# Kernel tuning notes

Measured on AMD Instinct MI355X. Metric: run time of the kernel, lower is better.

Reference implementation:

```python
import jax, jax.numpy as jnp
import numpy as np


def setup_inputs() -> dict:
    key = jax.random.key(0)
    k1, k2 = jax.random.split(key)
    B, L, D = 8, 2048, 128
    x1 = jax.random.normal(k1, (B, L, D), dtype=jnp.float32)
    x2 = jax.random.normal(k2, (B, L, D), dtype=jnp.float32)
    return {"x1": x1, "x2": x2}


def reference(x1, x2):
    # attention[b, i, j] = <x1[b,i,:], x2[b,j,:]>   -> [B, L1, L2]
    attention = jnp.einsum("bid,bjd->bij", x1, x2)
    # softmax over axis=1 (rows / L1) and axis=2 (cols / L2)
    w_att_1 = jax.nn.softmax(attention, axis=1)              # [B, L1, L2]
    w_att_2 = jnp.swapaxes(jax.nn.softmax(attention, axis=2), 1, 2)  # [B, L2, L1]
    # Dot(axes=1): contract the sequence axis 1
    in1_aligned = jnp.einsum("bij,bid->bjd", w_att_1, x1)    # [B, L2, D]
    in2_aligned = jnp.einsum("bji,bjd->bid", w_att_2, x2)    # [B, L1, D]
    # submult(a, b) = concat([a - b, a * b]); combined = concat([a, b, a-b, a*b])
    q1_combined = jnp.concatenate(
        [x1, in2_aligned, x1 - in2_aligned, x1 * in2_aligned], axis=-1)  # [B, L1, 4D]
    q2_combined = jnp.concatenate(
        [x2, in1_aligned, x2 - in1_aligned, x2 * in1_aligned], axis=-1)  # [B, L2, 4D]
    return q1_combined, q2_combined
```

## Files before the change

### kernel.cpp

```cpp
#include <hip/hip_runtime.h>


typedef __bf16    bf16;
typedef _Float16  f16;
typedef __bf16    bf16x4 __attribute__((ext_vector_type(4)));
typedef _Float16  f16x4  __attribute__((ext_vector_type(4)));
typedef __bf16    bf16x8 __attribute__((ext_vector_type(8)));
typedef _Float16  f16x8  __attribute__((ext_vector_type(8)));
typedef float     floatx4 __attribute__((ext_vector_type(4)));
typedef unsigned int uintx4 __attribute__((ext_vector_type(4)));

#define NB 8
#define SL 2048
#define TI 64
#define NT 32

#define F16SZ (NB * SL * 128 * 2)

#define SKV_S  136
#define SVT_S  32

#define OFF_VT   8704
#define GSPAN    16896
#define OFF_L    33792
#define LDS_BYTES 34048

__global__ __launch_bounds__(256)
void prepass_cvt(const float* __restrict__ x1, const float* __restrict__ x2,
                 char* __restrict__ ws)
{
    __shared__ float tile[64 * 129];
    const int tid = threadIdx.x;
    const int j0  = blockIdx.x * 64;
    const int b   = blockIdx.y;
    const int z   = blockIdx.z;
    const float* src = z ? x2 : x1;
    f16*  oF = (f16*) (ws + (size_t)z * F16SZ);
    bf16* oT = (bf16*)(ws + 2 * (size_t)F16SZ + (size_t)z * F16SZ);

    #pragma unroll
    for (int n = 0; n < 8; ++n) {
        int ci = n * 256 + tid;
        int row = ci >> 5, c4 = ci & 31;
        const float4 v = *(const float4*)(src + ((size_t)b * SL + j0 + row) * 128 + c4 * 4);
        tile[row * 129 + c4 * 4 + 0] = v.x;
        tile[row * 129 + c4 * 4 + 1] = v.y;
        tile[row * 129 + c4 * 4 + 2] = v.z;
        tile[row * 129 + c4 * 4 + 3] = v.w;
        f16x4 h; h[0] = (f16)v.x; h[1] = (f16)v.y; h[2] = (f16)v.z; h[3] = (f16)v.w;
        *(f16x4*)(oF + ((size_t)b * SL + j0 + row) * 128 + c4 * 4) = h;
    }
    __syncthreads();
    #pragma unroll
    for (int n = 0; n < 8; ++n) {
        int fi = n * 256 + tid;
        int jg = fi & 15, d = fi >> 4;
        bf16x4 o;
        #pragma unroll
        for (int i = 0; i < 4; ++i) o[i] = (bf16)tile[(jg * 4 + i) * 129 + d];
        *(bf16x4*)(oT + ((size_t)b * 128 + d) * SL + j0 + jg * 4) = o;
    }
}

__global__ __launch_bounds__(256, 2)
void soft_attn_align_mfma(const float* __restrict__ x1,
                          const float* __restrict__ x2,
                          const char* __restrict__ ws,
                          float* __restrict__ out)
{
    __shared__ __align__(16) char lds_raw[LDS_BYTES];

    const int tid  = threadIdx.x;
    const int lane = tid & 63;
    const int wv   = tid >> 6;
    const int g    = wv >> 1;
    const int rowbase = (wv & 1) * 32;
    const int lr   = lane & 15;
    const int lq   = lane >> 4;
    const int t128 = tid & 127;

    char* gb   = lds_raw + g * GSPAN;
    f16*   sKV  = (f16*) (gb);
    bf16*  sVT  = (bf16*)(gb + OFF_VT);
    float* aOut = (float*)(lds_raw);
    float* sL   = (float*)(lds_raw + OFF_L);

    const int i0  = blockIdx.x * TI;
    const int bi  = blockIdx.y;
    const int dir = blockIdx.z;

    const float* xq = dir ? x2 : x1;
    const f16*  x1f = (const f16*)(ws);
    const f16*  x2f = (const f16*)(ws + F16SZ);
    const bf16* x1T = (const bf16*)(ws + 2 * (size_t)F16SZ);
    const bf16* x2T = (const bf16*)(ws + 3 * (size_t)F16SZ);
    const f16*  xqf  = dir ? x2f : x1f;
    const f16*  xkvf = dir ? x1f : x2f;
    const bf16* xvT  = dir ? x1T : x2T;

    f16x8 aQ[2][4];
    #pragma unroll
    for (int rb = 0; rb < 2; ++rb) {
        const f16* qrow = xqf + ((size_t)bi * SL + i0 + rowbase + rb * 16 + lr) * 128;
        #pragma unroll
        for (int kk = 0; kk < 4; ++kk)
            aQ[rb][kk] = *(const f16x8*)(qrow + kk * 32 + lq * 8);
    }

    float   l_acc[2] = {0.f, 0.f};
    floatx4 Oacc[2][8];
    #pragma unroll
    for (int rb = 0; rb < 2; ++rb)
        #pragma unroll
        for (int nd = 0; nd < 8; ++nd) Oacc[rb][nd] = (floatx4){0.f, 0.f, 0.f, 0.f};

    const int rowK = t128 >> 4, colK = t128 & 15;
    const int dV0  = t128 >> 2, jcV  = t128 & 3;
    const f16*  kvf = xkvf + ((size_t)bi * SL + g * 1024 + rowK) * 128 + colK * 8;
    const bf16* vTf = xvT + ((size_t)bi * 128 + dV0) * SL + g * 1024 + jcV * 8;

    f16x8  kreg[4];
    bf16x8 vreg[4];
    {
        #pragma unroll
        for (int n = 0; n < 4; ++n) {
            kreg[n] = *(const f16x8*)(kvf + (size_t)n * 8 * 128);
            vreg[n] = *(const bf16x8*)(vTf + (size_t)n * 32 * SL);
        }
    }

    for (int t = 0; t < NT; ++t) {
        __syncthreads();

        #pragma unroll
        for (int n = 0; n < 4; ++n) {
            *(f16x8*) (sKV + (rowK + n * 8) * SKV_S + colK * 8) = kreg[n];
            *(bf16x8*)(sVT + (dV0 + n * 32) * SVT_S + jcV * 8)  = vreg[n];
        }
        __syncthreads();

        if (t < NT - 1) {
            const f16*  kb = kvf + (size_t)(t + 1) * 32 * 128;
            const bf16* vb = vTf + (size_t)(t + 1) * 32;
            #pragma unroll
            for (int n = 0; n < 4; ++n) {
                kreg[n] = *(const f16x8*)(kb + (size_t)n * 8 * 128);
                vreg[n] = *(const bf16x8*)(vb + (size_t)n * 32 * SL);
            }
        }

        floatx4 Sf[2][2];
        Sf[0][0] = (floatx4){0.f,0.f,0.f,0.f}; Sf[0][1] = (floatx4){0.f,0.f,0.f,0.f};
        Sf[1][0] = (floatx4){0.f,0.f,0.f,0.f}; Sf[1][1] = (floatx4){0.f,0.f,0.f,0.f};
        __builtin_amdgcn_s_setprio(1);
        #pragma unroll
        for (int kk = 0; kk < 4; ++kk) {
            f16x8 aK0 = *(const f16x8*)(sKV + (lr)      * SKV_S + kk * 32 + lq * 8);
            f16x8 aK1 = *(const f16x8*)(sKV + (16 + lr) * SKV_S + kk * 32 + lq * 8);
            Sf[0][0] = __builtin_amdgcn_mfma_f32_16x16x32_f16(aK0, aQ[0][kk], Sf[0][0], 0, 0, 0);
            Sf[0][1] = __builtin_amdgcn_mfma_f32_16x16x32_f16(aK1, aQ[0][kk], Sf[0][1], 0, 0, 0);
            Sf[1][0] = __builtin_amdgcn_mfma_f32_16x16x32_f16(aK0, aQ[1][kk], Sf[1][0], 0, 0, 0);
            Sf[1][1] = __builtin_amdgcn_mfma_f32_16x16x32_f16(aK1, aQ[1][kk], Sf[1][1], 0, 0, 0);
        }
        __builtin_amdgcn_s_setprio(0);

        bf16x8 aP[2];
        #pragma unroll
        for (int rb = 0; rb < 2; ++rb) {
            float p00 = __expf(Sf[rb][0][0]), p01 = __expf(Sf[rb][0][1]);
            float p02 = __expf(Sf[rb][0][2]), p03 = __expf(Sf[rb][0][3]);
            float p10 = __expf(Sf[rb][1][0]), p11 = __expf(Sf[rb][1][1]);
            float p12 = __expf(Sf[rb][1][2]), p13 = __expf(Sf[rb][1][3]);
            l_acc[rb] += ((p00 + p01) + (p02 + p03)) + ((p10 + p11) + (p12 + p13));

            unsigned int A0, B0, A1, B1;
            asm("v_cvt_pk_bf16_f32 %0, %1, %2" : "=v"(A0) : "v"(p00), "v"(p01));
            asm("v_cvt_pk_bf16_f32 %0, %1, %2" : "=v"(B0) : "v"(p02), "v"(p03));
            asm("v_cvt_pk_bf16_f32 %0, %1, %2" : "=v"(A1) : "v"(p10), "v"(p11));
            asm("v_cvt_pk_bf16_f32 %0, %1, %2" : "=v"(B1) : "v"(p12), "v"(p13));
            asm("v_permlane32_swap_b32 %0, %1" : "+v"(A0), "+v"(A1));
            asm("v_permlane16_swap_b32 %0, %1" : "+v"(A0), "+v"(A1));
            asm("v_permlane32_swap_b32 %0, %1" : "+v"(B0), "+v"(B1));
            asm("v_permlane16_swap_b32 %0, %1" : "+v"(B0), "+v"(B1));
            uintx4 fr; fr.x = A0; fr.y = B0; fr.z = A1; fr.w = B1;
            aP[rb] = __builtin_bit_cast(bf16x8, fr);
        }

        __builtin_amdgcn_s_setprio(1);
        #pragma unroll
        for (int nd = 0; nd < 8; ++nd) {
            bf16x8 bV = *(const bf16x8*)(sVT + (nd * 16 + lr) * SVT_S + lq * 8);
            Oacc[0][nd] = __builtin_amdgcn_mfma_f32_16x16x32_bf16(aP[0], bV, Oacc[0][nd], 0, 0, 0);
            Oacc[1][nd] = __builtin_amdgcn_mfma_f32_16x16x32_bf16(aP[1], bV, Oacc[1][nd], 0, 0, 0);
        }
        __builtin_amdgcn_s_setprio(0);
    }

    float l_row[2][4];
    #pragma unroll
    for (int rb = 0; rb < 2; ++rb) {
        float lv = l_acc[rb];
        lv += __shfl_xor(lv, 16, 64);
        lv += __shfl_xor(lv, 32, 64);
        #pragma unroll
        for (int r = 0; r < 4; ++r)
            l_row[rb][r] = __shfl(lv, lq * 4 + r, 64);
    }

    __syncthreads();

    if (g == 1) {
        #pragma unroll
        for (int rb = 0; rb < 2; ++rb)
            #pragma unroll
            for (int r = 0; r < 4; ++r) {
                int row = rowbase + rb * 16 + lq * 4 + r;
                #pragma unroll
                for (int nd = 0; nd < 8; ++nd)
                    aOut[row * 132 + nd * 16 + lr] = Oacc[rb][nd][r];
                if (lr == 0) sL[row] = l_row[rb][r];
            }
    }
    __syncthreads();
    if (g == 0) {
        #pragma unroll
        for (int rb = 0; rb < 2; ++rb)
            #pragma unroll
            for (int r = 0; r < 4; ++r) {
                int row = rowbase + rb * 16 + lq * 4 + r;
                float inv = 1.0f / (l_row[rb][r] + sL[row]);
                #pragma unroll
                for (int nd = 0; nd < 8; ++nd) {
                    int idx = row * 132 + nd * 16 + lr;
                    aOut[idx] = (Oacc[rb][nd][r] + aOut[idx]) * inv;
                }
            }
    }
    __syncthreads();

    float* outb = out + ((size_t)dir * NB * SL + (size_t)bi * SL + i0) * 512;
    #pragma unroll
    for (int k = 0; k < 8; ++k) {
        int s = tid + 256 * k;
        int r = s >> 5, c4 = s & 31;
        float4 a = *(const float4*)(aOut + r * 132 + c4 * 4);
        float4 q = *(const float4*)(xq + ((size_t)bi * SL + i0 + r) * 128 + c4 * 4);
        float4 d, m;
        d.x = q.x - a.x; d.y = q.y - a.y; d.z = q.z - a.z; d.w = q.w - a.w;
        m.x = q.x * a.x; m.y = q.y * a.y; m.z = q.z * a.z; m.w = q.w * a.w;
        float4* orow = (float4*)(outb + (size_t)r * 512);
        orow[c4]      = q;
        orow[32 + c4] = a;
        orow[64 + c4] = d;
        orow[96 + c4] = m;
    }
}

extern "C" void kernel_launch(void* const* d_in, const int* in_sizes, int n_in,
                              void* d_out, int out_size, void* d_ws, size_t ws_size,
                              hipStream_t stream) {
    const float* x1 = (const float*)d_in[0];
    const float* x2 = (const float*)d_in[1];
    float* out = (float*)d_out;
    (void)in_sizes; (void)n_in; (void)out_size; (void)ws_size;

    dim3 pgrid(SL / 64, NB, 2);
    prepass_cvt<<<pgrid, dim3(256), 0, stream>>>(x1, x2, (char*)d_ws);

    dim3 grid(SL / TI, NB, 2);
    soft_attn_align_mfma<<<grid, dim3(256), 0, stream>>>(x1, x2, (const char*)d_ws, out);
}
```

Measured before the change: 130.6 us.

## Double-buffer K/V tiles in LDS to halve barriers per iteration

Adds a second LDS buffer for the K and V^T tiles so the next tile is written to shared memory while the current one is consumed, with global prefetch moved two tiles ahead. This cuts the loop to one __syncthreads per iteration instead of two. In exchange the LDS footprint roughly doubles, to about 67 KB per block, which may limit how many blocks can reside per CU alongside the launch bound of 2.

```diff
diff --git a/kernel.cpp b/kernel.cpp
--- a/kernel.cpp
+++ b/kernel.cpp
@@ -20,10 +20,11 @@
 #define SKV_S  136
 #define SVT_S  32
 
+#define BUFH     16896
+#define GSPAN    33792
 #define OFF_VT   8704
-#define GSPAN    16896
-#define OFF_L    33792
-#define LDS_BYTES 34048
+#define OFF_L    67584
+#define LDS_BYTES 67840
 
 __global__ __launch_bounds__(256)
 void prepass_cvt(const float* __restrict__ x1, const float* __restrict__ x2,
@@ -79,9 +80,11 @@
     const int lq   = lane >> 4;
     const int t128 = tid & 127;
 
-    char* gb   = lds_raw + g * GSPAN;
-    f16*   sKV  = (f16*) (gb);
-    bf16*  sVT  = (bf16*)(gb + OFF_VT);
+    char* gb = lds_raw + g * GSPAN;
+    f16*  sKV0 = (f16*) (gb);
+    bf16* sVT0 = (bf16*)(gb + OFF_VT);
+    f16*  sKV1 = (f16*) (gb + BUFH);
+    bf16* sVT1 = (bf16*)(gb + BUFH + OFF_VT);
     float* aOut = (float*)(lds_raw);
     float* sL   = (float*)(lds_raw + OFF_L);
 
@@ -121,27 +124,40 @@
 
     f16x8  kreg[4];
     bf16x8 vreg[4];
-    {
-        #pragma unroll
-        for (int n = 0; n < 4; ++n) {
-            kreg[n] = *(const f16x8*)(kvf + (size_t)n * 8 * 128);
-            vreg[n] = *(const bf16x8*)(vTf + (size_t)n * 32 * SL);
-        }
-    }
+
+    #pragma unroll
+    for (int n = 0; n < 4; ++n) {
+        kreg[n] = *(const f16x8*)(kvf + (size_t)n * 8 * 128);
+        vreg[n] = *(const bf16x8*)(vTf + (size_t)n * 32 * SL);
+    }
+    #pragma unroll
+    for (int n = 0; n < 4; ++n) {
+        *(f16x8*) (sKV0 + (rowK + n * 8) * SKV_S + colK * 8) = kreg[n];
+        *(bf16x8*)(sVT0 + (dV0 + n * 32) * SVT_S + jcV * 8)  = vreg[n];
+    }
+    #pragma unroll
+    for (int n = 0; n < 4; ++n) {
+        kreg[n] = *(const f16x8*)(kvf + 32 * 128 + (size_t)n * 8 * 128);
+        vreg[n] = *(const bf16x8*)(vTf + 32 + (size_t)n * 32 * SL);
+    }
+    __syncthreads();
 
     for (int t = 0; t < NT; ++t) {
-        __syncthreads();
-
-        #pragma unroll
-        for (int n = 0; n < 4; ++n) {
-            *(f16x8*) (sKV + (rowK + n * 8) * SKV_S + colK * 8) = kreg[n];
-            *(bf16x8*)(sVT + (dV0 + n * 32) * SVT_S + jcV * 8)  = vreg[n];
-        }
-        __syncthreads();
+        f16*  sKVc = (t & 1) ? sKV1 : sKV0;
+        bf16* sVTc = (t & 1) ? sVT1 : sVT0;
+        f16*  sKVn = (t & 1) ? sKV0 : sKV1;
+        bf16* sVTn = (t & 1) ? sVT0 : sVT1;
 
         if (t < NT - 1) {
-            const f16*  kb = kvf + (size_t)(t + 1) * 32 * 128;
-            const bf16* vb = vTf + (size_t)(t + 1) * 32;
+            #pragma unroll
+            for (int n = 0; n < 4; ++n) {
+                *(f16x8*) (sKVn + (rowK + n * 8) * SKV_S + colK * 8) = kreg[n];
+                *(bf16x8*)(sVTn + (dV0 + n * 32) * SVT_S + jcV * 8)  = vreg[n];
+            }
+        }
+        if (t < NT - 2) {
+            const f16*  kb = kvf + (size_t)(t + 2) * 32 * 128;
+            const bf16* vb = vTf + (size_t)(t + 2) * 32;
             #pragma unroll
             for (int n = 0; n < 4; ++n) {
                 kreg[n] = *(const f16x8*)(kb + (size_t)n * 8 * 128);
@@ -155,8 +171,8 @@
         __builtin_amdgcn_s_setprio(1);
         #pragma unroll
         for (int kk = 0; kk < 4; ++kk) {
-            f16x8 aK0 = *(const f16x8*)(sKV + (lr)      * SKV_S + kk * 32 + lq * 8);
-            f16x8 aK1 = *(const f16x8*)(sKV + (16 + lr) * SKV_S + kk * 32 + lq * 8);
+            f16x8 aK0 = *(const f16x8*)(sKVc + (lr)      * SKV_S + kk * 32 + lq * 8);
+            f16x8 aK1 = *(const f16x8*)(sKVc + (16 + lr) * SKV_S + kk * 32 + lq * 8);
             Sf[0][0] = __builtin_amdgcn_mfma_f32_16x16x32_f16(aK0, aQ[0][kk], Sf[0][0], 0, 0, 0);
             Sf[0][1] = __builtin_amdgcn_mfma_f32_16x16x32_f16(aK1, aQ[0][kk], Sf[0][1], 0, 0, 0);
             Sf[1][0] = __builtin_amdgcn_mfma_f32_16x16x32_f16(aK0, aQ[1][kk], Sf[1][0], 0, 0, 0);
@@ -189,11 +205,13 @@
         __builtin_amdgcn_s_setprio(1);
         #pragma unroll
         for (int nd = 0; nd < 8; ++nd) {
-            bf16x8 bV = *(const bf16x8*)(sVT + (nd * 16 + lr) * SVT_S + lq * 8);
+            bf16x8 bV = *(const bf16x8*)(sVTc + (nd * 16 + lr) * SVT_S + lq * 8);
             Oacc[0][nd] = __builtin_amdgcn_mfma_f32_16x16x32_bf16(aP[0], bV, Oacc[0][nd], 0, 0, 0);
             Oacc[1][nd] = __builtin_amdgcn_mfma_f32_16x16x32_bf16(aP[1], bV, Oacc[1][nd], 0, 0, 0);
         }
         __builtin_amdgcn_s_setprio(0);
+
+        __syncthreads();
     }
 
     float l_row[2][4];
@@ -207,7 +225,6 @@
             l_row[rb][r] = __shfl(lv, lq * 4 + r, 64);
     }
 
-    __syncthreads();
 
     if (g == 1) {
         #pragma unroll
```

Measured after the change: 134.1 us. 1.03x slower.

## Split key sequence across four wave groups with 512-thread blocks and tree reduction

Applied to the files above, without the earlier changes.

Doubles the block to 512 threads so four wave-pair groups each process a quarter of the key/value sequence (16 tiles instead of 32), shortening the serial loop per block. Partial outputs and row sums are combined through a two-level LDS reduction with extra barriers. LDS usage doubles and launch bounds change to 512x4, which may limit occupancy and adds reduction overhead.

```diff
diff --git a/kernel.cpp b/kernel.cpp
--- a/kernel.cpp
+++ b/kernel.cpp
@@ -13,7 +13,7 @@
 #define NB 8
 #define SL 2048
 #define TI 64
-#define NT 32
+#define NT 16
 
 #define F16SZ (NB * SL * 128 * 2)
 
@@ -22,8 +22,9 @@
 
 #define OFF_VT   8704
 #define GSPAN    16896
-#define OFF_L    33792
-#define LDS_BYTES 34048
+#define OFF_LA   67584
+#define OFF_LB   67840
+#define LDS_BYTES 68096
 
 __global__ __launch_bounds__(256)
 void prepass_cvt(const float* __restrict__ x1, const float* __restrict__ x2,
@@ -62,7 +63,7 @@
     }
 }
 
-__global__ __launch_bounds__(256, 2)
+__global__ __launch_bounds__(512, 4)
 void soft_attn_align_mfma(const float* __restrict__ x1,
                           const float* __restrict__ x2,
                           const char* __restrict__ ws,
@@ -79,11 +80,13 @@
     const int lq   = lane >> 4;
     const int t128 = tid & 127;
 
-    char* gb   = lds_raw + g * GSPAN;
-    f16*   sKV  = (f16*) (gb);
-    bf16*  sVT  = (bf16*)(gb + OFF_VT);
-    float* aOut = (float*)(lds_raw);
-    float* sL   = (float*)(lds_raw + OFF_L);
+    char* gb  = lds_raw + g * GSPAN;
+    f16*  sKV = (f16*) (gb);
+    bf16* sVT = (bf16*)(gb + OFF_VT);
+    float* aOutA = (float*)(lds_raw);
+    float* aOutB = (float*)(lds_raw + 33792);
+    float* sLA   = (float*)(lds_raw + OFF_LA);
+    float* sLB   = (float*)(lds_raw + OFF_LB);
 
     const int i0  = blockIdx.x * TI;
     const int bi  = blockIdx.y;
@@ -116,8 +119,8 @@
 
     const int rowK = t128 >> 4, colK = t128 & 15;
     const int dV0  = t128 >> 2, jcV  = t128 & 3;
-    const f16*  kvf = xkvf + ((size_t)bi * SL + g * 1024 + rowK) * 128 + colK * 8;
-    const bf16* vTf = xvT + ((size_t)bi * 128 + dV0) * SL + g * 1024 + jcV * 8;
+    const f16*  kvf = xkvf + ((size_t)bi * SL + g * 512 + rowK) * 128 + colK * 8;
+    const bf16* vTf = xvT + ((size_t)bi * 128 + dV0) * SL + g * 512 + jcV * 8;
 
     f16x8  kreg[4];
     bf16x8 vreg[4];
@@ -209,7 +212,9 @@
 
     __syncthreads();
 
-    if (g == 1) {
+    if (g == 1 || g == 3) {
+        float* aO = (g == 1) ? aOutA : aOutB;
+        float* sl = (g == 1) ? sLA : sLB;
         #pragma unroll
         for (int rb = 0; rb < 2; ++rb)
             #pragma unroll
@@ -217,22 +222,50 @@
                 int row = rowbase + rb * 16 + lq * 4 + r;
                 #pragma unroll
                 for (int nd = 0; nd < 8; ++nd)
-                    aOut[row * 132 + nd * 16 + lr] = Oacc[rb][nd][r];
-                if (lr == 0) sL[row] = l_row[rb][r];
-            }
-    }
-    __syncthreads();
-    if (g == 0) {
+                    aO[row * 132 + nd * 16 + lr] = Oacc[rb][nd][r];
+                if (lr == 0) sl[row] = l_row[rb][r];
+            }
+    }
+    __syncthreads();
+    if (g == 0 || g == 2) {
+        float* aO = (g == 0) ? aOutA : aOutB;
+        float* sl = (g == 0) ? sLA : sLB;
         #pragma unroll
         for (int rb = 0; rb < 2; ++rb)
             #pragma unroll
             for (int r = 0; r < 4; ++r) {
                 int row = rowbase + rb * 16 + lq * 4 + r;
-                float inv = 1.0f / (l_row[rb][r] + sL[row]);
+                l_row[rb][r] += sl[row];
+                #pragma unroll
+                for (int nd = 0; nd < 8; ++nd)
+                    Oacc[rb][nd][r] += aO[row * 132 + nd * 16 + lr];
+            }
+    }
+    __syncthreads();
+    if (g == 2) {
+        #pragma unroll
+        for (int rb = 0; rb < 2; ++rb)
+            #pragma unroll
+            for (int r = 0; r < 4; ++r) {
+                int row = rowbase + rb * 16 + lq * 4 + r;
+                #pragma unroll
+                for (int nd = 0; nd < 8; ++nd)
+                    aOutA[row * 132 + nd * 16 + lr] = Oacc[rb][nd][r];
+                if (lr == 0) sLA[row] = l_row[rb][r];
+            }
+    }
+    __syncthreads();
+    if (g == 0) {
+        #pragma unroll
+        for (int rb = 0; rb < 2; ++rb)
+            #pragma unroll
+            for (int r = 0; r < 4; ++r) {
+                int row = rowbase + rb * 16 + lq * 4 + r;
+                float inv = 1.0f / (l_row[rb][r] + sLA[row]);
                 #pragma unroll
                 for (int nd = 0; nd < 8; ++nd) {
                     int idx = row * 132 + nd * 16 + lr;
-                    aOut[idx] = (Oacc[rb][nd][r] + aOut[idx]) * inv;
+                    aOutA[idx] = (Oacc[rb][nd][r] + aOutA[idx]) * inv;
                 }
             }
     }
@@ -240,10 +273,10 @@
 
     float* outb = out + ((size_t)dir * NB * SL + (size_t)bi * SL + i0) * 512;
     #pragma unroll
-    for (int k = 0; k < 8; ++k) {
-        int s = tid + 256 * k;
+    for (int k = 0; k < 4; ++k) {
+        int s = tid + 512 * k;
         int r = s >> 5, c4 = s & 31;
-        float4 a = *(const float4*)(aOut + r * 132 + c4 * 4);
+        float4 a = *(const float4*)(aOutA + r * 132 + c4 * 4);
         float4 q = *(const float4*)(xq + ((size_t)bi * SL + i0 + r) * 128 + c4 * 4);
         float4 d, m;
         d.x = q.x - a.x; d.y = q.y - a.y; d.z = q.z - a.z; d.w = q.w - a.w;
@@ -268,5 +301,5 @@
     prepass_cvt<<<pgrid, dim3(256), 0, stream>>>(x1, x2, (char*)d_ws);
 
     dim3 grid(SL / TI, NB, 2);
-    soft_attn_align_mfma<<<grid, dim3(256), 0, stream>>>(x1, x2, (const char*)d_ws, out);
+    soft_attn_align_mfma<<<grid, dim3(512), 0, stream>>>(x1, x2, (const char*)d_ws, out);
 }
```

Result: slower. 219.6 us (+68.1%).

## Halve query rows per block to raise occupancy and grid size

Applied to the files above, without the earlier changes.

Each block now handles 32 query rows instead of 64, so each wave computes one 16-row block rather than two. That halves the accumulator and Q-fragment registers and lets launch bounds request 4 blocks per SIMD instead of 2. The grid doubles, which improves latency hiding and load balance. In exchange every K/V tile is loaded from global memory and staged through LDS twice as often per query row, and the ratio of MFMA work to LDS traffic drops.

```diff
diff --git a/kernel.cpp b/kernel.cpp
--- a/kernel.cpp
+++ b/kernel.cpp
@@ -12,7 +12,7 @@
 
 #define NB 8
 #define SL 2048
-#define TI 64
+#define TI 32
 #define NT 32
 
 #define F16SZ (NB * SL * 128 * 2)
@@ -23,7 +23,7 @@
 #define OFF_VT   8704
 #define GSPAN    16896
 #define OFF_L    33792
-#define LDS_BYTES 34048
+#define LDS_BYTES 33920
 
 __global__ __launch_bounds__(256)
 void prepass_cvt(const float* __restrict__ x1, const float* __restrict__ x2,
@@ -62,7 +62,7 @@
     }
 }
 
-__global__ __launch_bounds__(256, 2)
+__global__ __launch_bounds__(256, 4)
 void soft_attn_align_mfma(const float* __restrict__ x1,
                           const float* __restrict__ x2,
                           const char* __restrict__ ws,
@@ -74,14 +74,14 @@
     const int lane = tid & 63;
     const int wv   = tid >> 6;
     const int g    = wv >> 1;
-    const int rowbase = (wv & 1) * 32;
+    const int rowbase = (wv & 1) * 16;
     const int lr   = lane & 15;
     const int lq   = lane >> 4;
     const int t128 = tid & 127;
 
-    char* gb   = lds_raw + g * GSPAN;
-    f16*   sKV  = (f16*) (gb);
-    bf16*  sVT  = (bf16*)(gb + OFF_VT);
+    char* gb  = lds_raw + g * GSPAN;
+    f16*  sKV = (f16*) (gb);
+    bf16* sVT = (bf16*)(gb + OFF_VT);
     float* aOut = (float*)(lds_raw);
     float* sL   = (float*)(lds_raw + OFF_L);
 
@@ -98,21 +98,18 @@
     const f16*  xkvf = dir ? x1f : x2f;
     const bf16* xvT  = dir ? x1T : x2T;
 
-    f16x8 aQ[2][4];
-    #pragma unroll
-    for (int rb = 0; rb < 2; ++rb) {
-        const f16* qrow = xqf + ((size_t)bi * SL + i0 + rowbase + rb * 16 + lr) * 128;
+    f16x8 aQ[4];
+    {
+        const f16* qrow = xqf + ((size_t)bi * SL + i0 + rowbase + lr) * 128;
         #pragma unroll
         for (int kk = 0; kk < 4; ++kk)
-            aQ[rb][kk] = *(const f16x8*)(qrow + kk * 32 + lq * 8);
-    }
-
-    float   l_acc[2] = {0.f, 0.f};
-    floatx4 Oacc[2][8];
-    #pragma unroll
-    for (int rb = 0; rb < 2; ++rb)
-        #pragma unroll
-        for (int nd = 0; nd < 8; ++nd) Oacc[rb][nd] = (floatx4){0.f, 0.f, 0.f, 0.f};
+            aQ[kk] = *(const f16x8*)(qrow + kk * 32 + lq * 8);
+    }
+
+    float   l_acc = 0.0f;
+    floatx4 Oacc[8];
+    #pragma unroll
+    for (int nd = 0; nd < 8; ++nd) Oacc[nd] = (floatx4){0.f, 0.f, 0.f, 0.f};
 
     const int rowK = t128 >> 4, colK = t128 & 15;
     const int dV0  = t128 >> 2, jcV  = t128 & 3;
@@ -149,98 +146,82 @@
             }
         }
 
-        floatx4 Sf[2][2];
-        Sf[0][0] = (floatx4){0.f,0.f,0.f,0.f}; Sf[0][1] = (floatx4){0.f,0.f,0.f,0.f};
-        Sf[1][0] = (floatx4){0.f,0.f,0.f,0.f}; Sf[1][1] = (floatx4){0.f,0.f,0.f,0.f};
+        floatx4 Sf0 = (floatx4){0.f, 0.f, 0.f, 0.f};
+        floatx4 Sf1 = (floatx4){0.f, 0.f, 0.f, 0.f};
         __builtin_amdgcn_s_setprio(1);
         #pragma unroll
         for (int kk = 0; kk < 4; ++kk) {
             f16x8 aK0 = *(const f16x8*)(sKV + (lr)      * SKV_S + kk * 32 + lq * 8);
             f16x8 aK1 = *(const f16x8*)(sKV + (16 + lr) * SKV_S + kk * 32 + lq * 8);
-            Sf[0][0] = __builtin_amdgcn_mfma_f32_16x16x32_f16(aK0, aQ[0][kk], Sf[0][0], 0, 0, 0);
-            Sf[0][1] = __builtin_amdgcn_mfma_f32_16x16x32_f16(aK1, aQ[0][kk], Sf[0][1], 0, 0, 0);
-            Sf[1][0] = __builtin_amdgcn_mfma_f32_16x16x32_f16(aK0, aQ[1][kk], Sf[1][0], 0, 0, 0);
-            Sf[1][1] = __builtin_amdgcn_mfma_f32_16x16x32_f16(aK1, aQ[1][kk], Sf[1][1], 0, 0, 0);
+            Sf0 = __builtin_amdgcn_mfma_f32_16x16x32_f16(aK0, aQ[kk], Sf0, 0, 0, 0);
+            Sf1 = __builtin_amdgcn_mfma_f32_16x16x32_f16(aK1, aQ[kk], Sf1, 0, 0, 0);
         }
         __builtin_amdgcn_s_setprio(0);
 
-        bf16x8 aP[2];
-        #pragma unroll
-        for (int rb = 0; rb < 2; ++rb) {
-            float p00 = __expf(Sf[rb][0][0]), p01 = __expf(Sf[rb][0][1]);
-            float p02 = __expf(Sf[rb][0][2]), p03 = __expf(Sf[rb][0][3]);
-            float p10 = __expf(Sf[rb][1][0]), p11 = __expf(Sf[rb][1][1]);
-            float p12 = __expf(Sf[rb][1][2]), p13 = __expf(Sf[rb][1][3]);
-            l_acc[rb] += ((p00 + p01) + (p02 + p03)) + ((p10 + p11) + (p12 + p13));
-
-            unsigned int A0, B0, A1, B1;
-            asm("v_cvt_pk_bf16_f32 %0, %1, %2" : "=v"(A0) : "v"(p00), "v"(p01));
-            asm("v_cvt_pk_bf16_f32 %0, %1, %2" : "=v"(B0) : "v"(p02), "v"(p03));
-            asm("v_cvt_pk_bf16_f32 %0, %1, %2" : "=v"(A1) : "v"(p10), "v"(p11));
-            asm("v_cvt_pk_bf16_f32 %0, %1, %2" : "=v"(B1) : "v"(p12), "v"(p13));
-            asm("v_permlane32_swap_b32 %0, %1" : "+v"(A0), "+v"(A1));
-            asm("v_permlane16_swap_b32 %0, %1" : "+v"(A0), "+v"(A1));
-            asm("v_permlane32_swap_b32 %0, %1" : "+v"(B0), "+v"(B1));
-            asm("v_permlane16_swap_b32 %0, %1" : "+v"(B0), "+v"(B1));
-            uintx4 fr; fr.x = A0; fr.y = B0; fr.z = A1; fr.w = B1;
-            aP[rb] = __builtin_bit_cast(bf16x8, fr);
-        }
+        float p00 = __expf(Sf0[0]), p01 = __expf(Sf0[1]);
+        float p02 = __expf(Sf0[2]), p03 = __expf(Sf0[3]);
+        float p10 = __expf(Sf1[0]), p11 = __expf(Sf1[1]);
+        float p12 = __expf(Sf1[2]), p13 = __expf(Sf1[3]);
+        l_acc += ((p00 + p01) + (p02 + p03)) + ((p10 + p11) + (p12 + p13));
+
+        unsigned int A0, B0, A1, B1;
+        asm("v_cvt_pk_bf16_f32 %0, %1, %2" : "=v"(A0) : "v"(p00), "v"(p01));
+        asm("v_cvt_pk_bf16_f32 %0, %1, %2" : "=v"(B0) : "v"(p02), "v"(p03));
+        asm("v_cvt_pk_bf16_f32 %0, %1, %2" : "=v"(A1) : "v"(p10), "v"(p11));
+        asm("v_cvt_pk_bf16_f32 %0, %1, %2" : "=v"(B1) : "v"(p12), "v"(p13));
+        asm("v_permlane32_swap_b32 %0, %1" : "+v"(A0), "+v"(A1));
+        asm("v_permlane16_swap_b32 %0, %1" : "+v"(A0), "+v"(A1));
+        asm("v_permlane32_swap_b32 %0, %1" : "+v"(B0), "+v"(B1));
+        asm("v_permlane16_swap_b32 %0, %1" : "+v"(B0), "+v"(B1));
+        uintx4 fr; fr.x = A0; fr.y = B0; fr.z = A1; fr.w = B1;
+        bf16x8 aP = __builtin_bit_cast(bf16x8, fr);
 
         __builtin_amdgcn_s_setprio(1);
         #pragma unroll
         for (int nd = 0; nd < 8; ++nd) {
             bf16x8 bV = *(const bf16x8*)(sVT + (nd * 16 + lr) * SVT_S + lq * 8);
-            Oacc[0][nd] = __builtin_amdgcn_mfma_f32_16x16x32_bf16(aP[0], bV, Oacc[0][nd], 0, 0, 0);
-            Oacc[1][nd] = __builtin_amdgcn_mfma_f32_16x16x32_bf16(aP[1], bV, Oacc[1][nd], 0, 0, 0);
+            Oacc[nd] = __builtin_amdgcn_mfma_f32_16x16x32_bf16(aP, bV, Oacc[nd], 0, 0, 0);
         }
         __builtin_amdgcn_s_setprio(0);
     }
 
-    float l_row[2][4];
-    #pragma unroll
-    for (int rb = 0; rb < 2; ++rb) {
-        float lv = l_acc[rb];
-        lv += __shfl_xor(lv, 16, 64);
-        lv += __shfl_xor(lv, 32, 64);
-        #pragma unroll
-        for (int r = 0; r < 4; ++r)
-            l_row[rb][r] = __shfl(lv, lq * 4 + r, 64);
-    }
+    l_acc += __shfl_xor(l_acc, 16, 64);
+    l_acc += __shfl_xor(l_acc, 32, 64);
+    float l_row[4];
+    #pragma unroll
+    for (int r = 0; r < 4; ++r)
+        l_row[r] = __shfl(l_acc, lq * 4 + r, 64);
 
     __syncthreads();
 
     if (g == 1) {
         #pragma unroll
-        for (int rb = 0; rb < 2; ++rb)
+        for (int r = 0; r < 4; ++r) {
+            int row = rowbase + lq * 4 + r;
             #pragma unroll
-            for (int r = 0; r < 4; ++r) {
-                int row = rowbase + rb * 16 + lq * 4 + r;
-                #pragma unroll
-                for (int nd = 0; nd < 8; ++nd)
-                    aOut[row * 132 + nd * 16 + lr] = Oacc[rb][nd][r];
-                if (lr == 0) sL[row] = l_row[rb][r];
+            for (int nd = 0; nd < 8; ++nd)
+                aOut[row * 132 + nd * 16 + lr] = Oacc[nd][r];
+            if (lr == 0) sL[row] = l_row[r];
+        }
+    }
+    __syncthreads();
+    if (g == 0) {
+        #pragma unroll
+        for (int r = 0; r < 4; ++r) {
+            int row = rowbase + lq * 4 + r;
+            float inv = 1.0f / (l_row[r] + sL[row]);
+            #pragma unroll
+            for (int nd = 0; nd < 8; ++nd) {
+                int idx = row * 132 + nd * 16 + lr;
+                aOut[idx] = (Oacc[nd][r] + aOut[idx]) * inv;
             }
-    }
-    __syncthreads();
-    if (g == 0) {
-        #pragma unroll
-        for (int rb = 0; rb < 2; ++rb)
-            #pragma unroll
-            for (int r = 0; r < 4; ++r) {
-                int row = rowbase + rb * 16 + lq * 4 + r;
-                float inv = 1.0f / (l_row[rb][r] + sL[row]);
-                #pragma unroll
-                for (int nd = 0; nd < 8; ++nd) {
-                    int idx = row * 132 + nd * 16 + lr;
-                    aOut[idx] = (Oacc[rb][nd][r] + aOut[idx]) * inv;
-                }
-            }
+        }
     }
     __syncthreads();
 
     float* outb = out + ((size_t)dir * NB * SL + (size_t)bi * SL + i0) * 512;
     #pragma unroll
-    for (int k = 0; k < 8; ++k) {
+    for (int k = 0; k < 4; ++k) {
         int s = tid + 256 * k;
         int r = s >> 5, c4 = s & 31;
         float4 a = *(const float4*)(aOut + r * 132 + c4 * 4);
```

Result: slower. 148.5 us (+13.7%).
